# Optimization experiments

Hardware: AMD Instinct MI355X
Metric: run time of the kernel (lower is better)

The kernel has to match this reference:

```python
import jax, jax.numpy as jnp
import numpy as np

DT = 0.005


def quat_product(q, r):
    # q, r: [B, 4] -> [B, 4]
    q0, q1, q2, q3 = q[:, 0], q[:, 1], q[:, 2], q[:, 3]
    r0, r1, r2, r3 = r[:, 0], r[:, 1], r[:, 2], r[:, 3]
    return jnp.stack([
        q0 * r0 - q1 * r1 - q2 * r2 - q3 * r3,
        q0 * r1 + q1 * r0 + q2 * r3 - q3 * r2,
        q0 * r2 - q1 * r3 + q2 * r0 + q3 * r1,
        q0 * r3 + q1 * r2 - q2 * r1 + q3 * r0,
    ], axis=1)


def quat_rotate(q, v):
    # q: [B, 4], v: [B, 3] -> [B, 3]
    q_conj = jnp.concatenate([q[:, :1], -q[:, 1:]], axis=1)
    v_quat = jnp.concatenate([jnp.zeros_like(v[:, :1]), v], axis=1)
    return quat_product(quat_product(q, v_quat), q_conj)[:, 1:]


def setup_inputs() -> dict:
    key = jax.random.key(0)
    ks = jax.random.split(key, 8)
    B, S, F, N = 1048576, 10, 6, 2097152
    return {
        "true_quaternions": jax.random.normal(ks[0], (B, 4), dtype=jnp.float32),
        "true_positions": jax.random.normal(ks[1], (B, 3), dtype=jnp.float32),
        "predicted_biases": jax.random.normal(ks[2], (B, 3), dtype=jnp.float32),
        "batch_X": jax.random.normal(ks[3], (B, S, F), dtype=jnp.float32),
        "positions_all": jax.random.normal(ks[4], (N, 3), dtype=jnp.float32),
        "velocities_all": jax.random.normal(ks[5], (N, 3), dtype=jnp.float32),
        "gravity_vector": jnp.array([0.0, 0.0, -9.81], dtype=jnp.float32),
        "indices": jax.random.randint(ks[6], (B,), 0, N, dtype=jnp.int64 if jax.config.jax_enable_x64 else jnp.int32),
        "sequence_length": 10,
    }


def reference(true_quaternions, true_positions, predicted_biases, batch_X,
              positions_all, velocities_all, gravity_vector, indices,
              sequence_length):
    # gather initial state: initial_index = max(idx - (seq_len - 1), 0)
    init_idx = jnp.maximum(indices - (sequence_length - 1), 0)
    p0 = positions_all[init_idx]   # [B, 3]
    v0 = velocities_all[init_idx]  # [B, 3]
    # bias-corrected acceleration from last timestep (disturbance = 0)
    acc = batch_X[:, -1, 0:3] - predicted_biases  # [B, 3]
    rotated = 0.5 * quat_rotate(true_quaternions, acc) * DT ** 2
    pred = p0 + v0 * DT + 0.5 * gravity_vector * DT ** 2 + rotated
    # Huber loss, delta = 1.0; per-sample mean over 3 coords then batch mean
    # equals elementwise mean over all B*3 elements
    d = pred - true_positions
    ad = jnp.abs(d)
    h = jnp.where(ad < 1.0, 0.5 * d * d, ad - 0.5)
    return jnp.mean(h)
```

## Files before the change

kernel.cpp:

```cpp
#include <hip/hip_runtime.h>
#include <math.h>

#define DT 0.005f
#define NTHREADS 256
#define NBLOCKS 2048
#define NBUCKET 32
#define ELEMS_PER_BLOCK 1024
#define ROUNDS 4

typedef float    fvec4 __attribute__((ext_vector_type(4)));
typedef float    fvec2 __attribute__((ext_vector_type(2)));
typedef unsigned uvec4 __attribute__((ext_vector_type(4)));

__device__ __forceinline__ fvec4 ntload4f(const float* p) {
    return __builtin_nontemporal_load(reinterpret_cast<const fvec4*>(p));
}
__device__ __forceinline__ fvec2 ntload2f(const float* p) {
    return __builtin_nontemporal_load(reinterpret_cast<const fvec2*>(p));
}
__device__ __forceinline__ float ntloadf(const float* p) {
    return __builtin_nontemporal_load(p);
}
__device__ __forceinline__ int ntloadi(const int* p) {
    return __builtin_nontemporal_load(p);
}
__device__ __forceinline__ uvec4 ntload4u(const unsigned* p) {
    return __builtin_nontemporal_load(reinterpret_cast<const uvec4*>(p));
}

__device__ __forceinline__ void stream_compute(
    const float* __restrict__ quat, const float* __restrict__ tpos,
    const float* __restrict__ bias, const float* __restrict__ batchX,
    int i, int SF, int last_off,
    float gx, float gy, float gz, float half_dt2,
    float& cx, float& cy, float& cz)
{
    fvec4 q = ntload4f(quat + (size_t)i * 4);
    const float* tp = tpos + (size_t)i * 3;
    float tpx = ntloadf(tp + 0), tpy = ntloadf(tp + 1), tpz = ntloadf(tp + 2);
    const float* bp = bias + (size_t)i * 3;
    float bx = ntloadf(bp + 0), by = ntloadf(bp + 1), bz = ntloadf(bp + 2);
    const float* xb = batchX + (size_t)i * SF + last_off;
    fvec2 a01 = ntload2f(xb);
    float ax = a01.x - bx;
    float ay = a01.y - by;
    float az = ntloadf(xb + 2) - bz;

    float t0 = -(q.y * ax + q.z * ay + q.w * az);
    float t1 =   q.x * ax + q.z * az - q.w * ay;
    float t2 =   q.x * ay - q.y * az + q.w * ax;
    float t3 =   q.x * az + q.y * ay - q.z * ax;
    float rx = -t0 * q.y + t1 * q.x - t2 * q.w + t3 * q.z;
    float ry = -t0 * q.z + t1 * q.w + t2 * q.x - t3 * q.y;
    float rz = -t0 * q.w - t1 * q.z + t2 * q.y + t3 * q.x;

    cx = half_dt2 * (gx + rx) - tpx;
    cy = half_dt2 * (gy + ry) - tpy;
    cz = half_dt2 * (gz + rz) - tpz;
}

__device__ __forceinline__ float huber3(float dx, float dy, float dz) {
    float adx = fabsf(dx), ady = fabsf(dy), adz = fabsf(dz);
    float h = (adx < 1.f) ? 0.5f * dx * dx : adx - 0.5f;
    h += (ady < 1.f) ? 0.5f * dy * dy : ady - 0.5f;
    h += (adz < 1.f) ? 0.5f * dz * dz : adz - 0.5f;
    return h;
}

__global__ __launch_bounds__(NTHREADS) void k1_bin(
    const float* __restrict__ quat,
    const float* __restrict__ tpos,
    const float* __restrict__ bias,
    const float* __restrict__ batchX,
    const float* __restrict__ grav,
    const int*   __restrict__ indices,
    const int*   __restrict__ seq_len_p,
    int SF, int shift,
    uvec4* __restrict__ pairs,
    int*   __restrict__ dirs)
{
    const int S = *seq_len_p;
    const int F = SF / S;
    const int last_off = (S - 1) * F;
    const float gx = grav[0], gy = grav[1], gz = grav[2];
    const float half_dt2 = 0.5f * DT * DT;

    __shared__ int   cnt[ROUNDS][4][NBUCKET];
    __shared__ int   offarr[ROUNDS][4][NBUCKET];
    __shared__ int   bstart[NBUCKET];
    __shared__ uvec4 stage[ELEMS_PER_BLOCK];

    const int tid  = threadIdx.x;
    const int wave = tid >> 6;
    const int lane = tid & 63;
    const unsigned long long ltmask = (1ull << lane) - 1ull;

    for (int k = tid; k < ROUNDS * 4 * NBUCKET; k += NTHREADS)
        ((int*)cnt)[k] = 0;
    __syncthreads();

    const int base = blockIdx.x * ELEMS_PER_BLOCK;

    int   idxv[ROUNDS], bckt[ROUNDS], rnk[ROUNDS];
    float cxv[ROUNDS], cyv[ROUNDS], czv[ROUNDS];

    #pragma unroll
    for (int r = 0; r < ROUNDS; ++r) {
        const int i = base + r * NTHREADS + tid;
        int idx = ntloadi(indices + i) - (S - 1);
        if (idx < 0) idx = 0;
        idxv[r] = idx;
        int b = idx >> shift; if (b > NBUCKET - 1) b = NBUCKET - 1;
        bckt[r] = b;

        unsigned long long mask = ~0ull;
        #pragma unroll
        for (int k = 0; k < 5; ++k) {
            unsigned long long bm = __ballot((b >> k) & 1);
            mask &= ((b >> k) & 1) ? bm : ~bm;
        }
        rnk[r] = __popcll(mask & ltmask);
        if (rnk[r] == 0) cnt[r][wave][b] = __popcll(mask);

        stream_compute(quat, tpos, bias, batchX, i, SF, last_off,
                       gx, gy, gz, half_dt2, cxv[r], cyv[r], czv[r]);
    }
    __syncthreads();

    if (tid < NBUCKET) {
        int b = tid, off = 0;
        #pragma unroll
        for (int r = 0; r < ROUNDS; ++r)
            #pragma unroll
            for (int w = 0; w < 4; ++w) {
                offarr[r][w][b] = off;
                off += cnt[r][w][b];
            }
        dirs[blockIdx.x * NBUCKET + b] = off;
        cnt[0][0][b] = off;
    }
    __syncthreads();
    if (tid == 0) {
        int s = 0;
        #pragma unroll
        for (int b = 0; b < NBUCKET; ++b) { bstart[b] = s; s += cnt[0][0][b]; }
    }
    __syncthreads();

    #pragma unroll
    for (int r = 0; r < ROUNDS; ++r) {
        int slot = bstart[bckt[r]] + offarr[r][wave][bckt[r]] + rnk[r];
        uvec4 v;
        v.x = (unsigned)idxv[r];
        v.y = __float_as_uint(cxv[r]);
        v.z = __float_as_uint(cyv[r]);
        v.w = __float_as_uint(czv[r]);
        stage[slot] = v;
    }
    __syncthreads();

    #pragma unroll
    for (int r = 0; r < ROUNDS; ++r)
        pairs[(size_t)base + r * NTHREADS + tid] = stage[r * NTHREADS + tid];
}

__global__ __launch_bounds__(NTHREADS) void k2_gather(
    const float* __restrict__ pos_all,
    const float* __restrict__ vel_all,
    const uvec4* __restrict__ pairs,
    const int*   __restrict__ dirs,
    float* __restrict__ partials)
{
    const int r = blockIdx.x & 7;
    const int j = blockIdx.x >> 3;
    const int tid = threadIdx.x;

    __shared__ int dcnt[8][NBUCKET];
    __shared__ int segSrc[8];
    __shared__ int segCum[9];
    __shared__ float wsum[NTHREADS / 64];

    {
        int s = tid >> 5, bb = tid & (NBUCKET - 1);
        dcnt[s][bb] = dirs[(j * 8 + s) * NBUCKET + bb];
    }
    __syncthreads();

    float hsum = 0.f;

    for (int phase = 0; phase < NBUCKET / 8; ++phase) {
        const int b = r + 8 * phase;

        if (tid < 8) {
            int s = tid, st = 0;
            for (int bb = 0; bb < b; ++bb) st += dcnt[s][bb];
            segSrc[s] = (j * 8 + s) * ELEMS_PER_BLOCK + st;
            segCum[s] = dcnt[s][b];
        }
        __syncthreads();
        if (tid == 0) {
            int c = 0;
            #pragma unroll
            for (int s = 0; s < 8; ++s) { int l = segCum[s]; segCum[s] = c; c += l; }
            segCum[8] = c;
        }
        __syncthreads();

        const int tot = segCum[8];
        for (int m = tid; m < tot; m += NTHREADS) {
            int s = 0;
            #pragma unroll
            for (int k = 1; k < 8; ++k) s += (m >= segCum[k]);
            uvec4 pr = ntload4u(
                reinterpret_cast<const unsigned*>(pairs + segSrc[s] + (m - segCum[s])));
            int idx = (int)pr.x;
            const float* pp = pos_all + (size_t)idx * 3;
            const float* vp = vel_all + (size_t)idx * 3;
            float cx = __uint_as_float(pr.y);
            float cy = __uint_as_float(pr.z);
            float cz = __uint_as_float(pr.w);
            hsum += huber3(pp[0] + vp[0] * DT + cx,
                           pp[1] + vp[1] * DT + cy,
                           pp[2] + vp[2] * DT + cz);
        }
        __syncthreads();
    }

    for (int off = 32; off > 0; off >>= 1)
        hsum += __shfl_down(hsum, off);

    int lane = tid & 63, wid = tid >> 6;
    if (lane == 0) wsum[wid] = hsum;
    __syncthreads();
    if (tid == 0) {
        float s = 0.f;
        for (int w = 0; w < NTHREADS / 64; ++w) s += wsum[w];
        partials[blockIdx.x] = s;
    }
}

__global__ __launch_bounds__(NTHREADS) void pos_loss_partial(
    const float* __restrict__ quat,
    const float* __restrict__ tpos,
    const float* __restrict__ bias,
    const float* __restrict__ batchX,
    const float* __restrict__ pos_all,
    const float* __restrict__ vel_all,
    const float* __restrict__ grav,
    const int*   __restrict__ indices,
    const int*   __restrict__ seq_len_p,
    int B, int SF,
    float* __restrict__ partials)
{
    const int S = *seq_len_p;
    const int F = SF / S;
    const int last_off = (S - 1) * F;
    const float gx = grav[0], gy = grav[1], gz = grav[2];
    const float half_dt2 = 0.5f * DT * DT;

    float hsum = 0.f;

    for (int i = blockIdx.x * blockDim.x + threadIdx.x; i < B;
         i += gridDim.x * blockDim.x) {
        int idx = ntloadi(indices + i) - (S - 1);
        if (idx < 0) idx = 0;
        const float* pp = pos_all + (size_t)idx * 3;
        const float* vp = vel_all + (size_t)idx * 3;
        float p0x = pp[0], p0y = pp[1], p0z = pp[2];
        float v0x = vp[0], v0y = vp[1], v0z = vp[2];

        float cx, cy, cz;
        stream_compute(quat, tpos, bias, batchX, i, SF, last_off,
                       gx, gy, gz, half_dt2, cx, cy, cz);

        hsum += huber3(p0x + v0x * DT + cx,
                       p0y + v0y * DT + cy,
                       p0z + v0z * DT + cz);
    }

    for (int off = 32; off > 0; off >>= 1)
        hsum += __shfl_down(hsum, off);

    __shared__ float wsum[NTHREADS / 64];
    int lane = threadIdx.x & 63;
    int wid  = threadIdx.x >> 6;
    if (lane == 0) wsum[wid] = hsum;
    __syncthreads();
    if (threadIdx.x == 0) {
        float s = 0.f;
        for (int w = 0; w < NTHREADS / 64; ++w) s += wsum[w];
        partials[blockIdx.x] = s;
    }
}

__global__ __launch_bounds__(NTHREADS) void pos_loss_finish(
    const float* __restrict__ partials, int nb, float inv_cnt,
    float* __restrict__ out)
{
    float s = 0.f;
    for (int i = threadIdx.x; i < nb; i += NTHREADS) s += partials[i];
    for (int off = 32; off > 0; off >>= 1)
        s += __shfl_down(s, off);
    __shared__ float wsum[NTHREADS / 64];
    int lane = threadIdx.x & 63;
    int wid  = threadIdx.x >> 6;
    if (lane == 0) wsum[wid] = s;
    __syncthreads();
    if (threadIdx.x == 0) {
        float tot = 0.f;
        for (int w = 0; w < NTHREADS / 64; ++w) tot += wsum[w];
        out[0] = tot * inv_cnt;
    }
}

extern "C" void kernel_launch(void* const* d_in, const int* in_sizes, int n_in,
                              void* d_out, int out_size, void* d_ws, size_t ws_size,
                              hipStream_t stream) {
    const float* quat    = (const float*)d_in[0];
    const float* tpos    = (const float*)d_in[1];
    const float* bias    = (const float*)d_in[2];
    const float* batchX  = (const float*)d_in[3];
    const float* pos_all = (const float*)d_in[4];
    const float* vel_all = (const float*)d_in[5];
    const float* grav    = (const float*)d_in[6];
    const int*   indices = (const int*)d_in[7];
    const int*   seqlen  = (const int*)d_in[8];

    const int B  = in_sizes[0] / 4;
    const int SF = in_sizes[3] / B;
    const int N  = in_sizes[4] / 3;

    float inv_cnt = (float)(1.0 / (3.0 * (double)B));
    float* outp = (float*)d_out;

    const int nseg = B / ELEMS_PER_BLOCK;
    uvec4* pairs    = (uvec4*)d_ws;
    int*   dirs     = (int*)((char*)d_ws + (size_t)B * 16);
    float* partials = (float*)((char*)d_ws + (size_t)B * 16 +
                               (size_t)nseg * NBUCKET * 4);
    const size_t need = (size_t)B * 16 + (size_t)nseg * NBUCKET * 4 +
                        (size_t)nseg * 4 + 256;

    const bool pipe_ok = (B % (ELEMS_PER_BLOCK * 8) == 0) && (ws_size >= need) &&
                         (N > NBUCKET);

    if (pipe_ok) {
        int shift = 0;
        while (((long long)(N - 1) >> shift) >= NBUCKET) ++shift;

        k1_bin<<<nseg, NTHREADS, 0, stream>>>(
            quat, tpos, bias, batchX, grav, indices, seqlen,
            SF, shift, pairs, dirs);
        k2_gather<<<nseg, NTHREADS, 0, stream>>>(
            pos_all, vel_all, pairs, dirs, partials);
        pos_loss_finish<<<1, NTHREADS, 0, stream>>>(
            partials, nseg, inv_cnt, outp);
    } else {
        float* fpart = (float*)d_ws;
        pos_loss_partial<<<NBLOCKS, NTHREADS, 0, stream>>>(
            quat, tpos, bias, batchX, pos_all, vel_all, grav, indices, seqlen,
            B, SF, fpart);
        pos_loss_finish<<<1, NTHREADS, 0, stream>>>(
            fpart, NBLOCKS, inv_cnt, outp);
    }
}
```

Measured before the change: 59.56 us.

## Precompute packed p+v*DT table so the gather reads one aligned 16-byte row

Adds extra blocks to the binning kernel that stream over all N positions and velocities and write a packed float4 table holding p + DT*v. The gather kernel then issues one aligned 16-byte load per sample instead of six scattered scalar loads from two arrays. The aim is fewer gather transactions and cache lines per sample. In exchange it adds a full streaming pass over 2M rows (about 48MB read, 32MB written) plus a larger workspace requirement, which could outweigh the savings when B is only half of N.

```diff
diff --git a/kernel.cpp b/kernel.cpp
--- a/kernel.cpp
+++ b/kernel.cpp
@@ -7,6 +7,7 @@
 #define NBUCKET 32
 #define ELEMS_PER_BLOCK 1024
 #define ROUNDS 4
+#define NPREP 1024
 
 typedef float    fvec4 __attribute__((ext_vector_type(4)));
 typedef float    fvec2 __attribute__((ext_vector_type(2)));
@@ -67,18 +68,39 @@
     return h;
 }
 
-__global__ __launch_bounds__(NTHREADS) void k1_bin(
+__global__ __launch_bounds__(NTHREADS) void k1_bin_prep(
     const float* __restrict__ quat,
     const float* __restrict__ tpos,
     const float* __restrict__ bias,
     const float* __restrict__ batchX,
+    const float* __restrict__ pos_all,
+    const float* __restrict__ vel_all,
     const float* __restrict__ grav,
     const int*   __restrict__ indices,
     const int*   __restrict__ seq_len_p,
-    int SF, int shift,
+    int SF, int shift, int nseg, int N,
     uvec4* __restrict__ pairs,
-    int*   __restrict__ dirs)
-{
+    int*   __restrict__ dirs,
+    float* __restrict__ w4)
+{
+    const int tid = threadIdx.x;
+
+    if ((int)blockIdx.x >= nseg) {
+        const int pb = blockIdx.x - nseg;
+        const int stride = NPREP * NTHREADS;
+        for (int n = pb * NTHREADS + tid; n < N; n += stride) {
+            const float* pp = pos_all + (size_t)n * 3;
+            const float* vp = vel_all + (size_t)n * 3;
+            fvec4 r;
+            r.x = pp[0] + DT * vp[0];
+            r.y = pp[1] + DT * vp[1];
+            r.z = pp[2] + DT * vp[2];
+            r.w = 0.f;
+            *reinterpret_cast<fvec4*>(w4 + (size_t)n * 4) = r;
+        }
+        return;
+    }
+
     const int S = *seq_len_p;
     const int F = SF / S;
     const int last_off = (S - 1) * F;
@@ -90,7 +112,6 @@
     __shared__ int   bstart[NBUCKET];
     __shared__ uvec4 stage[ELEMS_PER_BLOCK];
 
-    const int tid  = threadIdx.x;
     const int wave = tid >> 6;
     const int lane = tid & 63;
     const unsigned long long ltmask = (1ull << lane) - 1ull;
@@ -164,9 +185,8 @@
         pairs[(size_t)base + r * NTHREADS + tid] = stage[r * NTHREADS + tid];
 }
 
-__global__ __launch_bounds__(NTHREADS) void k2_gather(
-    const float* __restrict__ pos_all,
-    const float* __restrict__ vel_all,
+__global__ __launch_bounds__(NTHREADS) void k2_gather_w(
+    const float* __restrict__ w4,
     const uvec4* __restrict__ pairs,
     const int*   __restrict__ dirs,
     float* __restrict__ partials)
@@ -214,14 +234,10 @@
             uvec4 pr = ntload4u(
                 reinterpret_cast<const unsigned*>(pairs + segSrc[s] + (m - segCum[s])));
             int idx = (int)pr.x;
-            const float* pp = pos_all + (size_t)idx * 3;
-            const float* vp = vel_all + (size_t)idx * 3;
-            float cx = __uint_as_float(pr.y);
-            float cy = __uint_as_float(pr.z);
-            float cz = __uint_as_float(pr.w);
-            hsum += huber3(pp[0] + vp[0] * DT + cx,
-                           pp[1] + vp[1] * DT + cy,
-                           pp[2] + vp[2] * DT + cz);
+            fvec4 wv = *reinterpret_cast<const fvec4*>(w4 + (size_t)idx * 4);
+            hsum += huber3(wv.x + __uint_as_float(pr.y),
+                           wv.y + __uint_as_float(pr.z),
+                           wv.z + __uint_as_float(pr.w));
         }
         __syncthreads();
     }
@@ -334,12 +350,17 @@
     float* outp = (float*)d_out;
 
     const int nseg = B / ELEMS_PER_BLOCK;
-    uvec4* pairs    = (uvec4*)d_ws;
-    int*   dirs     = (int*)((char*)d_ws + (size_t)B * 16);
-    float* partials = (float*)((char*)d_ws + (size_t)B * 16 +
-                               (size_t)nseg * NBUCKET * 4);
-    const size_t need = (size_t)B * 16 + (size_t)nseg * NBUCKET * 4 +
-                        (size_t)nseg * 4 + 256;
+
+    size_t off_pairs = 0;
+    size_t off_dirs  = off_pairs + (size_t)B * 16;
+    size_t off_part  = off_dirs + (size_t)nseg * NBUCKET * 4;
+    size_t off_w4    = (off_part + (size_t)nseg * 4 + 255) & ~(size_t)255;
+    size_t need      = off_w4 + (size_t)N * 16;
+
+    uvec4* pairs    = (uvec4*)((char*)d_ws + off_pairs);
+    int*   dirs     = (int*)((char*)d_ws + off_dirs);
+    float* partials = (float*)((char*)d_ws + off_part);
+    float* w4       = (float*)((char*)d_ws + off_w4);
 
     const bool pipe_ok = (B % (ELEMS_PER_BLOCK * 8) == 0) && (ws_size >= need) &&
                          (N > NBUCKET);
@@ -348,11 +369,11 @@
         int shift = 0;
         while (((long long)(N - 1) >> shift) >= NBUCKET) ++shift;
 
-        k1_bin<<<nseg, NTHREADS, 0, stream>>>(
-            quat, tpos, bias, batchX, grav, indices, seqlen,
-            SF, shift, pairs, dirs);
-        k2_gather<<<nseg, NTHREADS, 0, stream>>>(
-            pos_all, vel_all, pairs, dirs, partials);
+        k1_bin_prep<<<nseg + NPREP, NTHREADS, 0, stream>>>(
+            quat, tpos, bias, batchX, pos_all, vel_all, grav, indices, seqlen,
+            SF, shift, nseg, N, pairs, dirs, w4);
+        k2_gather_w<<<nseg, NTHREADS, 0, stream>>>(
+            w4, pairs, dirs, partials);
         pos_loss_finish<<<1, NTHREADS, 0, stream>>>(
             partials, nseg, inv_cnt, outp);
     } else {
```

Result: slower. 66.62 us (+11.8%).
